# Performance work log

Measured on AMD Instinct MI355X. Metric: run time of the kernel, lower is better.

The kernel has to match this reference:

```python
import jax, jax.numpy as jnp
import numpy as np

MARGIN = 0.5
BETA = 0.0
K = 5

def setup_inputs() -> dict:
    key = jax.random.key(0)
    k1, k2 = jax.random.split(key)
    n, d, n_classes = 4096, 512, 512
    inputs = jax.random.normal(k1, (n, d), dtype=jnp.float32)
    # L2-normalize as is standard for similarity-based DML embeddings
    inputs = inputs / jnp.linalg.norm(inputs, axis=1, keepdims=True)
    targets = jax.random.randint(k2, (n,), 0, n_classes, dtype=jnp.int64)
    return {"inputs": inputs, "targets": targets}

def reference(inputs, targets):
    n = inputs.shape[0]
    sim = inputs @ inputs.T                      # [n, n] similarity matrix
    same = targets[:, None] == targets[None, :]  # [n, n] same-class mask
    eye = jnp.eye(n, dtype=bool)
    pos_mask = same & ~eye                       # positive pairs (off-diagonal)
    neg_mask = ~same                             # negative pairs
    # margin_loss (hinge on similarity): pos -> [margin + beta - s]_+, neg -> [margin + s - beta]_+
    pos_l = jnp.maximum(MARGIN + BETA - sim, 0.0)
    neg_l = jnp.maximum(MARGIN + sim - BETA, 0.0)
    valid = pos_mask | neg_mask
    pair_loss = jnp.where(pos_mask, pos_l, neg_l)  # per-pair loss where valid
    num_of_zeros = jnp.sum(valid & (pair_loss == 0.0))
    # top-(4K) over the multiset of all valid pair losses (== topk of concat(pos_loss, neg_loss))
    masked = jnp.where(valid, pair_loss, -jnp.inf).reshape(-1)
    top_loss, _ = jax.lax.top_k(masked, 4 * K)
    loss = jnp.mean(top_loss)
    mean_pos_sim = jnp.sum(jnp.where(pos_mask, sim, 0.0)) / jnp.sum(pos_mask)
    mean_neg_sim = jnp.sum(jnp.where(neg_mask, sim, 0.0)) / jnp.sum(neg_mask)
    # NOTE: the original swaps the names: it returns mean(pos_sim) as `mean_neg_sim` and vice versa.
    return (loss, num_of_zeros, mean_pos_sim, mean_neg_sim)
```

## Files before the change

kernel.cpp:

```cpp
#include <hip/hip_runtime.h>
#include <hip/hip_fp16.h>

constexpr int N = 4096;
constexpr int D = 512;
constexpr int NT = 32;
constexpr int NBLK = NT * (NT + 1) / 2;
constexpr float SENT = -1e30f;

typedef _Float16 f16x8 __attribute__((ext_vector_type(8)));
typedef float f32x4 __attribute__((ext_vector_type(4)));

#define BAR() asm volatile("s_barrier" ::: "memory")
#define WAITV8() asm volatile("s_waitcnt vmcnt(8)" ::: "memory")
#define WAITV0() asm volatile("s_waitcnt vmcnt(0)" ::: "memory")

__device__ __forceinline__ void load_lds16(const _Float16* g, _Float16* l) {
  __builtin_amdgcn_global_load_lds(
      (const __attribute__((address_space(1))) void*)g,
      (__attribute__((address_space(3))) void*)l, 16, 0, 0);
}

__device__ __forceinline__ void ins10(float (&t)[10], float v) {
#pragma unroll
  for (int k = 9; k > 0; k--) t[k] = fmaxf(t[k], fminf(v, t[k - 1]));
  t[0] = fmaxf(t[0], v);
}

constexpr int TOP10_OFF = 10560;
constexpr int XH_OFF = 31744;

__global__ void prep_kernel(const float4* __restrict__ X4,
                            ushort4* __restrict__ Xh4) {
  int gid = blockIdx.x * 256 + threadIdx.x;
  float4 v = X4[gid];
  ushort4 o;
  o.x = __half_as_ushort(__float2half_rn(v.x));
  o.y = __half_as_ushort(__float2half_rn(v.y));
  o.z = __half_as_ushort(__float2half_rn(v.z));
  o.w = __half_as_ushort(__float2half_rn(v.w));
  Xh4[gid] = o;
}

__global__ __launch_bounds__(256, 2) void gemm_stats_kernel(
    const _Float16* __restrict__ Xh, const int* __restrict__ tgt,
    float* __restrict__ slots, float* __restrict__ top10g) {
  float* blk_sumv = slots;
  float* blk_sump = slots + NBLK;
  unsigned* blk_cntv = (unsigned*)(slots + 2 * NBLK);
  unsigned* blk_cntp = (unsigned*)(slots + 3 * NBLK);
  unsigned* blk_zero = (unsigned*)(slots + 4 * NBLK);

  __shared__ _Float16 As[2 * 128 * 64];
  __shared__ _Float16 Bs[2 * 128 * 64];
  __shared__ float Lf[256 * 10];
  __shared__ int tA[128], tB[128];
  __shared__ float redf[2][4];
  __shared__ unsigned redu[3][4];

  int tid = threadIdx.x;

  int id = blockIdx.x, br = 0;
  while (id >= (NT - br)) { id -= (NT - br); br++; }
  int bc = br + id;

  if (tid < 128) tA[tid] = tgt[br * 128 + tid];
  else           tB[tid - 128] = tgt[bc * 128 + (tid - 128)];

  int lane = tid & 63, wave = tid >> 6;
  int wm = (wave >> 1) << 6;
  int wn = (wave & 1) << 6;
  int lrow = lane & 15;
  int q4 = lane >> 4;
  int x7 = lrow & 7;
  int quad4 = q4 * 4;

  int srow[4], scol[4], sdst[4];
#pragma unroll
  for (int i = 0; i < 4; i++) {
    int C = (i * 4 + wave) * 64 + lane;
    int row = C >> 3, p = C & 7;
    srow[i] = row;
    scol[i] = (p ^ (row & 7)) * 8;
    sdst[i] = (i * 4 + wave) * 512;
  }
  const _Float16* Arow = Xh + (size_t)(br * 128) * D;
  const _Float16* Brow = Xh + (size_t)(bc * 128) * D;

  auto issue = [&](int k0, int sel) {
#pragma unroll
    for (int i = 0; i < 4; i++) {
      load_lds16(Arow + srow[i] * D + k0 + scol[i], As + sel * 8192 + sdst[i]);
      load_lds16(Brow + srow[i] * D + k0 + scol[i], Bs + sel * 8192 + sdst[i]);
    }
  };

  f32x4 acc[4][4] = {};

  __syncthreads();
  issue(0, 0);

#pragma unroll
  for (int it = 0; it < 8; ++it) {
    int sel = it & 1;
    if (it > 0) BAR();
    if (it < 7) {
      issue((it + 1) * 64, sel ^ 1);
      WAITV8();
    } else {
      WAITV0();
    }
    BAR();
#pragma unroll
    for (int ks = 0; ks < 64; ks += 32) {
      int c0 = ks >> 3;
      f16x8 af[4], bf[4];
#pragma unroll
      for (int mi = 0; mi < 4; mi++)
        af[mi] = *(const f16x8*)&As[sel * 8192 + (wm + mi * 16 + lrow) * 64 +
                                    ((c0 + q4) ^ x7) * 8];
#pragma unroll
      for (int ni = 0; ni < 4; ni++)
        bf[ni] = *(const f16x8*)&Bs[sel * 8192 + (wn + ni * 16 + lrow) * 64 +
                                    ((c0 + q4) ^ x7) * 8];
#pragma unroll
      for (int mi = 0; mi < 4; mi++)
#pragma unroll
        for (int ni = 0; ni < 4; ni++)
          acc[mi][ni] = __builtin_amdgcn_mfma_f32_16x16x32_f16(
              af[mi], bf[ni], acc[mi][ni], 0, 0, 0);
    }
  }

  int ti[4][4], tj[4];
#pragma unroll
  for (int ni = 0; ni < 4; ni++) tj[ni] = tB[wn + ni * 16 + lrow];
#pragma unroll
  for (int mi = 0; mi < 4; mi++)
#pragma unroll
    for (int r = 0; r < 4; r++) ti[mi][r] = tA[wm + mi * 16 + quad4 + r];

  float lsv = 0.f, lsp = 0.f;
  unsigned lcv = 0, lcp = 0, lz = 0;
  int ibase = br * 128 + wm + quad4;
  int jbase = bc * 128 + wn + lrow;

  float t10[10];
#pragma unroll
  for (int k = 0; k < 10; k++) t10[k] = SENT;

#pragma unroll
  for (int mi = 0; mi < 4; mi++)
#pragma unroll
    for (int ni = 0; ni < 4; ni++)
#pragma unroll
      for (int r = 0; r < 4; r++) {
        float s = acc[mi][ni][r];
        int i = ibase + mi * 16 + r;
        int j = jbase + ni * 16;
        bool valid = j > i;
        bool pos = valid && (ti[mi][r] == tj[ni]);
        float t = pos ? -s : s;
        float loss = fmaxf(0.5f + t, 0.0f);
        if (valid) { lsv += s; lcv++; if (loss == 0.0f) lz++; }
        if (pos) { lsp += s; lcp++; }
        ins10(t10, valid ? loss : SENT);
      }

#pragma unroll
  for (int o = 32; o > 0; o >>= 1) {
    lsv += __shfl_down(lsv, o);
    lsp += __shfl_down(lsp, o);
    lcv += __shfl_down(lcv, o);
    lcp += __shfl_down(lcp, o);
    lz  += __shfl_down(lz, o);
  }
  if (lane == 0) {
    redf[0][wave] = lsv; redf[1][wave] = lsp;
    redu[0][wave] = lcv; redu[1][wave] = lcp; redu[2][wave] = lz;
  }

#pragma unroll
  for (int k = 0; k < 10; k++) Lf[tid * 10 + k] = t10[k];
  for (int s2 = 128; s2 >= 1; s2 >>= 1) {
    __syncthreads();
    if (tid < s2) {
#pragma unroll
      for (int k = 0; k < 10; k++) ins10(t10, Lf[(tid + s2) * 10 + k]);
#pragma unroll
      for (int k = 0; k < 10; k++) Lf[tid * 10 + k] = t10[k];
    }
  }
  __syncthreads();

  if (tid == 0) {
    int b = blockIdx.x;
    blk_sumv[b] = redf[0][0] + redf[0][1] + redf[0][2] + redf[0][3];
    blk_sump[b] = redf[1][0] + redf[1][1] + redf[1][2] + redf[1][3];
    blk_cntv[b] = redu[0][0] + redu[0][1] + redu[0][2] + redu[0][3];
    blk_cntp[b] = redu[1][0] + redu[1][1] + redu[1][2] + redu[1][3];
    blk_zero[b] = redu[2][0] + redu[2][1] + redu[2][2] + redu[2][3];
#pragma unroll
    for (int k = 0; k < 10; k++) top10g[b * 10 + k] = t10[k];
  }
}

__global__ void finalize_kernel(const float* __restrict__ slots,
                                const float* __restrict__ top10g,
                                float* __restrict__ out) {
  const float* blk_sumv = slots;
  const float* blk_sump = slots + NBLK;
  const unsigned* blk_cntv = (const unsigned*)(slots + 2 * NBLK);
  const unsigned* blk_cntp = (const unsigned*)(slots + 3 * NBLK);
  const unsigned* blk_zero = (const unsigned*)(slots + 4 * NBLK);

  __shared__ float Lf[256 * 10];
  __shared__ float rf[2][4];
  __shared__ unsigned ru[3][4];

  int tid = threadIdx.x;
  int lane = tid & 63, wave = tid >> 6;

  float sv = 0.f, sp = 0.f;
  unsigned cv = 0, cp = 0, zz = 0;
  for (int b = tid; b < NBLK; b += 256) {
    sv += blk_sumv[b]; sp += blk_sump[b];
    cv += blk_cntv[b]; cp += blk_cntp[b]; zz += blk_zero[b];
  }
#pragma unroll
  for (int o = 32; o > 0; o >>= 1) {
    sv += __shfl_down(sv, o);
    sp += __shfl_down(sp, o);
    cv += __shfl_down(cv, o);
    cp += __shfl_down(cp, o);
    zz += __shfl_down(zz, o);
  }
  if (lane == 0) {
    rf[0][wave] = sv; rf[1][wave] = sp;
    ru[0][wave] = cv; ru[1][wave] = cp; ru[2][wave] = zz;
  }

  float t[10];
#pragma unroll
  for (int k = 0; k < 10; k++) t[k] = SENT;
  for (int g = tid; g < NBLK * 10; g += 256) ins10(t, top10g[g]);
#pragma unroll
  for (int k = 0; k < 10; k++) Lf[tid * 10 + k] = t[k];

  for (int s = 128; s >= 1; s >>= 1) {
    __syncthreads();
    if (tid < s) {
#pragma unroll
      for (int k = 0; k < 10; k++) ins10(t, Lf[(tid + s) * 10 + k]);
#pragma unroll
      for (int k = 0; k < 10; k++) Lf[tid * 10 + k] = t[k];
    }
  }
  __syncthreads();

  if (tid == 0) {
    float topsum = 0.f;
#pragma unroll
    for (int k = 0; k < 10; k++) topsum += t[k];
    float tsv = rf[0][0] + rf[0][1] + rf[0][2] + rf[0][3];
    float tsp = rf[1][0] + rf[1][1] + rf[1][2] + rf[1][3];
    unsigned tcv = ru[0][0] + ru[0][1] + ru[0][2] + ru[0][3];
    unsigned tcp = ru[1][0] + ru[1][1] + ru[1][2] + ru[1][3];
    unsigned tzz = ru[2][0] + ru[2][1] + ru[2][2] + ru[2][3];
    out[0] = topsum * 0.1f;
    out[1] = (float)(2u * tzz);
    out[2] = tsp / (float)tcp;
    out[3] = (tsv - tsp) / (float)(tcv - tcp);
  }
}

extern "C" void kernel_launch(void* const* d_in, const int* in_sizes, int n_in,
                              void* d_out, int out_size, void* d_ws, size_t ws_size,
                              hipStream_t stream) {
  const float* X = (const float*)d_in[0];
  const int* tgt = (const int*)d_in[1];
  float* out = (float*)d_out;
  char* ws = (char*)d_ws;

  float* slots = (float*)ws;
  float* top10g = (float*)(ws + TOP10_OFF);
  _Float16* Xh = (_Float16*)(ws + XH_OFF);

  prep_kernel<<<(N * D / 4) / 256, 256, 0, stream>>>((const float4*)X,
                                                     (ushort4*)Xh);
  gemm_stats_kernel<<<NBLK, 256, 0, stream>>>(Xh, tgt, slots, top10g);
  finalize_kernel<<<1, 256, 0, stream>>>(slots, top10g, out);
}
```

Before: 109.5 us.

## Fuse finalize into GEMM kernel via last-block atomic and shuffle top-k merge

Removes the separate finalize kernel launch by having each block increment a global counter, with the last-arriving block doing the final reduction. It also replaces the per-block LDS tree reduction of top-10 lists, which needed many barriers, with a wave-level xor-shuffle merge followed by a small cross-wave merge. This cuts one kernel launch and the barrier-heavy LDS reduction. In exchange it adds an atomic plus threadfence per block and a serial tail in the last block.

```diff
diff --git a/kernel.cpp b/kernel.cpp
--- a/kernel.cpp
+++ b/kernel.cpp
@@ -26,12 +26,26 @@
   t[0] = fmaxf(t[0], v);
 }
 
+__device__ __forceinline__ void wave_merge10(float (&t)[10]) {
+#pragma unroll
+  for (int ofs = 1; ofs < 64; ofs <<= 1) {
+    float o[10];
+#pragma unroll
+    for (int k = 0; k < 10; k++) o[k] = __shfl_xor(t[k], ofs);
+#pragma unroll
+    for (int k = 0; k < 10; k++) ins10(t, o[k]);
+  }
+}
+
 constexpr int TOP10_OFF = 10560;
+constexpr int DONE_OFF = 31680;
 constexpr int XH_OFF = 31744;
 
 __global__ void prep_kernel(const float4* __restrict__ X4,
-                            ushort4* __restrict__ Xh4) {
+                            ushort4* __restrict__ Xh4,
+                            unsigned* __restrict__ done) {
   int gid = blockIdx.x * 256 + threadIdx.x;
+  if (gid == 0) *done = 0u;
   float4 v = X4[gid];
   ushort4 o;
   o.x = __half_as_ushort(__float2half_rn(v.x));
@@ -43,7 +57,8 @@
 
 __global__ __launch_bounds__(256, 2) void gemm_stats_kernel(
     const _Float16* __restrict__ Xh, const int* __restrict__ tgt,
-    float* __restrict__ slots, float* __restrict__ top10g) {
+    float* __restrict__ slots, float* __restrict__ top10g,
+    unsigned* __restrict__ done, float* __restrict__ out) {
   float* blk_sumv = slots;
   float* blk_sump = slots + NBLK;
   unsigned* blk_cntv = (unsigned*)(slots + 2 * NBLK);
@@ -52,10 +67,11 @@
 
   __shared__ _Float16 As[2 * 128 * 64];
   __shared__ _Float16 Bs[2 * 128 * 64];
-  __shared__ float Lf[256 * 10];
   __shared__ int tA[128], tB[128];
   __shared__ float redf[2][4];
   __shared__ unsigned redu[3][4];
+  __shared__ float wt[4][10];
+  __shared__ int lastFlag;
 
   int tid = threadIdx.x;
 
@@ -174,51 +190,48 @@
     lcp += __shfl_down(lcp, o);
     lz  += __shfl_down(lz, o);
   }
+  wave_merge10(t10);
   if (lane == 0) {
     redf[0][wave] = lsv; redf[1][wave] = lsp;
     redu[0][wave] = lcv; redu[1][wave] = lcp; redu[2][wave] = lz;
-  }
-
-#pragma unroll
-  for (int k = 0; k < 10; k++) Lf[tid * 10 + k] = t10[k];
-  for (int s2 = 128; s2 >= 1; s2 >>= 1) {
-    __syncthreads();
-    if (tid < s2) {
-#pragma unroll
-      for (int k = 0; k < 10; k++) ins10(t10, Lf[(tid + s2) * 10 + k]);
-#pragma unroll
-      for (int k = 0; k < 10; k++) Lf[tid * 10 + k] = t10[k];
+#pragma unroll
+    for (int k = 0; k < 10; k++) wt[wave][k] = t10[k];
+  }
+  __syncthreads();
+
+  if (wave == 0) {
+    float m10[10];
+#pragma unroll
+    for (int k = 0; k < 10; k++) m10[k] = (lane < 4) ? wt[lane][k] : SENT;
+#pragma unroll
+    for (int ofs = 1; ofs < 4; ofs <<= 1) {
+      float o[10];
+#pragma unroll
+      for (int k = 0; k < 10; k++) o[k] = __shfl_xor(m10[k], ofs);
+#pragma unroll
+      for (int k = 0; k < 10; k++) ins10(m10, o[k]);
+    }
+    if (lane == 0) {
+      int b = blockIdx.x;
+      blk_sumv[b] = redf[0][0] + redf[0][1] + redf[0][2] + redf[0][3];
+      blk_sump[b] = redf[1][0] + redf[1][1] + redf[1][2] + redf[1][3];
+      blk_cntv[b] = redu[0][0] + redu[0][1] + redu[0][2] + redu[0][3];
+      blk_cntp[b] = redu[1][0] + redu[1][1] + redu[1][2] + redu[1][3];
+      blk_zero[b] = redu[2][0] + redu[2][1] + redu[2][2] + redu[2][3];
+#pragma unroll
+      for (int k = 0; k < 10; k++) top10g[b * 10 + k] = m10[k];
     }
   }
   __syncthreads();
 
   if (tid == 0) {
-    int b = blockIdx.x;
-    blk_sumv[b] = redf[0][0] + redf[0][1] + redf[0][2] + redf[0][3];
-    blk_sump[b] = redf[1][0] + redf[1][1] + redf[1][2] + redf[1][3];
-    blk_cntv[b] = redu[0][0] + redu[0][1] + redu[0][2] + redu[0][3];
-    blk_cntp[b] = redu[1][0] + redu[1][1] + redu[1][2] + redu[1][3];
-    blk_zero[b] = redu[2][0] + redu[2][1] + redu[2][2] + redu[2][3];
-#pragma unroll
-    for (int k = 0; k < 10; k++) top10g[b * 10 + k] = t10[k];
-  }
-}
-
-__global__ void finalize_kernel(const float* __restrict__ slots,
-                                const float* __restrict__ top10g,
-                                float* __restrict__ out) {
-  const float* blk_sumv = slots;
-  const float* blk_sump = slots + NBLK;
-  const unsigned* blk_cntv = (const unsigned*)(slots + 2 * NBLK);
-  const unsigned* blk_cntp = (const unsigned*)(slots + 3 * NBLK);
-  const unsigned* blk_zero = (const unsigned*)(slots + 4 * NBLK);
-
-  __shared__ float Lf[256 * 10];
-  __shared__ float rf[2][4];
-  __shared__ unsigned ru[3][4];
-
-  int tid = threadIdx.x;
-  int lane = tid & 63, wave = tid >> 6;
+    __threadfence();
+    unsigned old = atomicAdd(done, 1u);
+    lastFlag = (old == NBLK - 1);
+  }
+  __syncthreads();
+  if (!lastFlag) return;
+  __threadfence();
 
   float sv = 0.f, sp = 0.f;
   unsigned cv = 0, cp = 0, zz = 0;
@@ -235,37 +248,36 @@
     zz += __shfl_down(zz, o);
   }
   if (lane == 0) {
-    rf[0][wave] = sv; rf[1][wave] = sp;
-    ru[0][wave] = cv; ru[1][wave] = cp; ru[2][wave] = zz;
-  }
-
-  float t[10];
-#pragma unroll
-  for (int k = 0; k < 10; k++) t[k] = SENT;
-  for (int g = tid; g < NBLK * 10; g += 256) ins10(t, top10g[g]);
-#pragma unroll
-  for (int k = 0; k < 10; k++) Lf[tid * 10 + k] = t[k];
-
-  for (int s = 128; s >= 1; s >>= 1) {
-    __syncthreads();
-    if (tid < s) {
-#pragma unroll
-      for (int k = 0; k < 10; k++) ins10(t, Lf[(tid + s) * 10 + k]);
-#pragma unroll
-      for (int k = 0; k < 10; k++) Lf[tid * 10 + k] = t[k];
-    }
-  }
+    redf[0][wave] = sv; redf[1][wave] = sp;
+    redu[0][wave] = cv; redu[1][wave] = cp; redu[2][wave] = zz;
+  }
+
+  float f10[10];
+#pragma unroll
+  for (int k = 0; k < 10; k++) f10[k] = SENT;
+  for (int g = tid; g < NBLK * 10; g += 256) ins10(f10, top10g[g]);
+  wave_merge10(f10);
+  if (lane == 0)
+#pragma unroll
+    for (int k = 0; k < 10; k++) wt[wave][k] = f10[k];
   __syncthreads();
 
   if (tid == 0) {
+    float m10[10];
+#pragma unroll
+    for (int k = 0; k < 10; k++) m10[k] = wt[0][k];
+#pragma unroll
+    for (int w = 1; w < 4; w++)
+#pragma unroll
+      for (int k = 0; k < 10; k++) ins10(m10, wt[w][k]);
     float topsum = 0.f;
 #pragma unroll
-    for (int k = 0; k < 10; k++) topsum += t[k];
-    float tsv = rf[0][0] + rf[0][1] + rf[0][2] + rf[0][3];
-    float tsp = rf[1][0] + rf[1][1] + rf[1][2] + rf[1][3];
-    unsigned tcv = ru[0][0] + ru[0][1] + ru[0][2] + ru[0][3];
-    unsigned tcp = ru[1][0] + ru[1][1] + ru[1][2] + ru[1][3];
-    unsigned tzz = ru[2][0] + ru[2][1] + ru[2][2] + ru[2][3];
+    for (int k = 0; k < 10; k++) topsum += m10[k];
+    float tsv = redf[0][0] + redf[0][1] + redf[0][2] + redf[0][3];
+    float tsp = redf[1][0] + redf[1][1] + redf[1][2] + redf[1][3];
+    unsigned tcv = redu[0][0] + redu[0][1] + redu[0][2] + redu[0][3];
+    unsigned tcp = redu[1][0] + redu[1][1] + redu[1][2] + redu[1][3];
+    unsigned tzz = redu[2][0] + redu[2][1] + redu[2][2] + redu[2][3];
     out[0] = topsum * 0.1f;
     out[1] = (float)(2u * tzz);
     out[2] = tsp / (float)tcp;
@@ -283,10 +295,10 @@
 
   float* slots = (float*)ws;
   float* top10g = (float*)(ws + TOP10_OFF);
+  unsigned* done = (unsigned*)(ws + DONE_OFF);
   _Float16* Xh = (_Float16*)(ws + XH_OFF);
 
   prep_kernel<<<(N * D / 4) / 256, 256, 0, stream>>>((const float4*)X,
-                                                     (ushort4*)Xh);
-  gemm_stats_kernel<<<NBLK, 256, 0, stream>>>(Xh, tgt, slots, top10g);
-  finalize_kernel<<<1, 256, 0, stream>>>(slots, top10g, out);
-}
+                                                     (ushort4*)Xh, done);
+  gemm_stats_kernel<<<NBLK, 256, 0, stream>>>(Xh, tgt, slots, top10g, done, out);
+}
```

New measurement: 116.2 us. 6.2% more time.
